# Optimization experiments

Measured on AMD Instinct MI355X. Metric: run time of the kernel, lower is better.

## Reference

```python
import jax, jax.numpy as jnp
import numpy as np

EPS = 0.01       # perturbation radius (constructor arg)
MEAN = 0.1307    # MNIST normalize constants from the 'else' branch
SIGMA = 0.3081


def _get_bound(v, eps):
    # torch get_bound detaches eps before taking |.| and summing
    r = jnp.sum(jnp.abs(jax.lax.stop_gradient(eps)), axis=-1)
    return v + r, v - r


def _relu_zono(v, eps):
    # v: [N], eps: [N, E]. Append one fresh (zero) error column, as the torch code does.
    n = v.shape[0]
    eps = jnp.concatenate([eps, jnp.zeros((n, 1), eps.dtype)], axis=-1)  # [N, E+1]
    u, l = _get_bound(v, eps)
    denom = u - l  # = 2*sum|eps| >= 0; guard against 0 for non-crossing rows
    # slopes are created as Parameters = u/(u-l) on the first pass (detached leaf)
    slope = jax.lax.stop_gradient(u / jnp.where(denom == 0, 1.0, denom))
    # at init slope == base = u/(u-l), so the slope <= base branch is taken
    term = (1.0 - slope) * u * 0.5
    crossing = (u > 0) & (l < 0)
    dead = u <= 0
    # torch uses slope.data * values.data for the linear part, + term (term carries grad)
    v_cross = jax.lax.stop_gradient(slope * v) + term
    v_new = jnp.where(dead, 0.0, jnp.where(crossing, v_cross, v))
    eps_cross = jnp.concatenate([slope[:, None] * eps[:, :-1], term[:, None]], axis=-1)
    eps_new = jnp.where(dead[:, None], 0.0, jnp.where(crossing[:, None], eps_cross, eps))
    return v_new, eps_new


def _forward(inputs, W1, b1, W2, b2, W3, b3):
    # initial zonotope build (faithful to source: values = u + l, radii = values - l = u)
    upper = jnp.minimum(inputs + EPS, 1.0)   # upper - relu(upper - 1)
    lower = jnp.maximum(inputs - EPS, 0.0)   # relu(lower)
    values = upper + lower
    eps = jnp.diag((values - lower).flatten())  # [D, D]
    # Normalize layer (the 'else' branch)
    values = (values - MEAN) / SIGMA
    eps = eps / SIGMA
    # Flatten
    v = values.flatten()
    # Linear -> ReLU -> Linear -> ReLU -> Linear
    v = W1 @ v + b1
    eps = W1 @ eps
    v, eps = _relu_zono(v, eps)
    v = W2 @ v + b2
    eps = W2 @ eps
    v, eps = _relu_zono(v, eps)
    v = W3 @ v + b3
    eps = W3 @ eps
    u, l = _get_bound(v, eps)
    return u, l


def setup_inputs() -> dict:
    key = jax.random.key(0)
    ks = jax.random.split(key, 7)
    D, H, O = 1024, 4096, 10
    inputs = jax.random.uniform(ks[0], (1, 1, 32, 32), jnp.float32)
    W1 = jax.random.normal(ks[1], (H, D), jnp.float32) / np.float32(np.sqrt(D))
    b1 = jax.random.normal(ks[2], (H,), jnp.float32) * 0.01
    W2 = jax.random.normal(ks[3], (H, H), jnp.float32) / np.float32(np.sqrt(H))
    b2 = jax.random.normal(ks[4], (H,), jnp.float32) * 0.01
    W3 = jax.random.normal(ks[5], (O, H), jnp.float32) / np.float32(np.sqrt(H))
    b3 = jax.random.normal(ks[6], (O,), jnp.float32) * 0.01
    return {"inputs": inputs, "W1": W1, "b1": b1, "W2": W2, "b2": b2, "W3": W3, "b3": b3}


def reference(inputs, W1, b1, W2, b2, W3, b3):
    return _forward(inputs, W1, b1, W2, b2, W3, b3)
```

## Files before the change

### kernel.cpp

```cpp
#include <hip/hip_runtime.h>
#include <math.h>

#define ZEPS  0.01f
#define ZMEAN 0.1307f
#define ZSIGMA 0.3081f

constexpr int D = 1024, H = 4096, O = 10;

using short8 = __attribute__((ext_vector_type(8))) short;
using f32x4  = __attribute__((ext_vector_type(4))) float;
typedef unsigned short ushort_t;

__device__ inline unsigned short f2bf(float x) {
    unsigned int u = __float_as_uint(x);
    u += 0x7FFFu + ((u >> 16) & 1u);
    return (unsigned short)(u >> 16);
}
__device__ inline float bf2f(unsigned short h) {
    return __uint_as_float(((unsigned int)h) << 16);
}

__device__ inline unsigned int f2bf2_fast(float a, float b) {
    unsigned int ua = __float_as_uint(a) + 0x8000u;
    unsigned int ub = __float_as_uint(b) + 0x8000u;
    return (ua >> 16) | (ub & 0xFFFF0000u);
}

__device__ inline void gl_lds16(const void* g, void* l) {
    __builtin_amdgcn_global_load_lds(
        (const __attribute__((address_space(1))) unsigned int*)g,
        (__attribute__((address_space(3))) unsigned int*)l, 16, 0, 0);
}

__device__ inline float zval(float xv) {
    float up = fminf(xv + ZEPS, 1.f);
    float lo = fmaxf(xv - ZEPS, 0.f);
    return (up + lo - ZMEAN) / ZSIGMA;
}
__device__ inline float zdia(float xv) {
    return fminf(xv + ZEPS, 1.f) / ZSIGMA;
}

__device__ inline void relu_params(float v, float r, float& vout, float& aout, float& tout) {
    float u = v + r, l = v - r;
    float denom = u - l;
    float slope = u / (denom == 0.f ? 1.f : denom);
    float term = (1.f - slope) * u * 0.5f;
    bool dead = (u <= 0.f);
    bool crossing = (u > 0.f) && (l < 0.f);
    vout = dead ? 0.f : (crossing ? (slope * v + term) : v);
    aout = dead ? 0.f : (crossing ? slope : 1.f);
    tout = (!dead && crossing) ? term : 0.f;
}

__global__ __launch_bounds__(256) void k_layer1(const float* __restrict__ W1, const float* __restrict__ b1,
                                                const float* __restrict__ x,
                                                float* __restrict__ v1p, float* __restrict__ a1,
                                                float* __restrict__ t1) {
    int wid = threadIdx.x >> 6, lane = threadIdx.x & 63;
    int i = blockIdx.x * 4 + wid;
    const float* row = W1 + (size_t)i * D;
    float sv = 0.f, sr = 0.f;
#pragma unroll
    for (int it = 0; it < 4; ++it) {
        int j = it * 256 + lane * 4;
        float4 w = *(const float4*)&row[j];
        float4 xx = *(const float4*)&x[j];
        sv += w.x * zval(xx.x) + w.y * zval(xx.y) + w.z * zval(xx.z) + w.w * zval(xx.w);
        sr += fabsf(w.x) * zdia(xx.x) + fabsf(w.y) * zdia(xx.y) +
              fabsf(w.z) * zdia(xx.z) + fabsf(w.w) * zdia(xx.w);
    }
#pragma unroll
    for (int m = 1; m <= 32; m <<= 1) {
        sv += __shfl_xor(sv, m, 64);
        sr += __shfl_xor(sr, m, 64);
    }
    if (lane == 0) {
        float vo, ao, to;
        relu_params(sv + b1[i], sr, vo, ao, to);
        v1p[i] = vo; a1[i] = ao; t1[i] = to;
    }
}

__global__ __launch_bounds__(256) void k_scaleT(const float* __restrict__ W1, const float* __restrict__ a1,
                                                const float* __restrict__ x,
                                                ushort_t* __restrict__ W1sT) {
    __shared__ float tile[32][33];
    int j0 = blockIdx.x * 32, k0 = blockIdx.y * 32;
    int r = threadIdx.x >> 3;
    int c = (threadIdx.x & 7) * 4;
    float4 w = *(const float4*)&W1[(size_t)(k0 + r) * D + j0 + c];
    float4 xx = *(const float4*)&x[j0 + c];
    float a = a1[k0 + r];
    tile[r][c + 0] = a * w.x * zdia(xx.x);
    tile[r][c + 1] = a * w.y * zdia(xx.y);
    tile[r][c + 2] = a * w.z * zdia(xx.z);
    tile[r][c + 3] = a * w.w * zdia(xx.w);
    __syncthreads();
    ushort4 o;
    o.x = f2bf(tile[c + 0][r]);
    o.y = f2bf(tile[c + 1][r]);
    o.z = f2bf(tile[c + 2][r]);
    o.w = f2bf(tile[c + 3][r]);
    *(ushort4*)&W1sT[(size_t)(j0 + r) * H + k0 + c] = o;
}

#define GBK 64
__global__ __launch_bounds__(256) void k_gemm_mfma(const float* __restrict__ A,
                                                   const ushort_t* __restrict__ B,
                                                   const float* __restrict__ v1p,
                                                   const float* __restrict__ t1,
                                                   ushort_t* __restrict__ C,
                                                   float* __restrict__ vpart,
                                                   float* __restrict__ tpart) {
    const int N = D, K = H;
    __shared__ __align__(16) ushort_t As[2][128 * GBK];
    __shared__ __align__(16) ushort_t Bs[2][128 * GBK];
    __shared__ float vt[2048], tt[2048];
    int b = blockIdx.x;
    int u = b & 7, v = b >> 3;
    int z = u >> 2;
    int y = (u & 3) * 8 + (v >> 3);
    int xb = v & 7;
    int tid = threadIdx.x;
    int wave = tid >> 6, lane = tid & 63;
    int bm = y * 128, bn = xb * 128;
    int kbeg = z * (K / 2);
    ushort_t* Cz = C + (size_t)z * ((size_t)H * D);
    int wm = (wave >> 1) * 64, wn = (wave & 1) * 64;

    int srow = lane >> 3, sc = lane & 7, scp = sc ^ srow;
    int r15 = lane & 15, quad = lane >> 4, key = r15 & 7;
    int rowg = tid >> 3, ch = tid & 7;
    int aswz = ch ^ (rowg & 7);

    const int S = (K / 2) / GBK;

    float4 pa[4][2];
    float sv[4] = {0.f, 0.f, 0.f, 0.f}, st[4] = {0.f, 0.f, 0.f, 0.f};

    auto issueA = [&](int s) {
#pragma unroll
        for (int g = 0; g < 4; ++g) {
            const float* ap = &A[(size_t)(bm + g * 32 + rowg) * K + kbeg + s * GBK + ch * 8];
            pa[g][0] = *(const float4*)ap;
            pa[g][1] = *(const float4*)(ap + 4);
        }
    };
    auto issueB = [&](int s, int buf) {
#pragma unroll
        for (int g = 0; g < 2; ++g) {
            int row = wave * 32 + g * 16;
            (void)row;
        }
#pragma unroll
        for (int g = 0; g < 4; ++g) {
            int row = wave * 32 + g * 8;
            gl_lds16(&B[(size_t)(bn + row + srow) * K + kbeg + s * GBK + scp * 8], &Bs[buf][row * GBK]);
        }
    };
    auto cvtwrite = [&](int s, int buf) {
        if ((s & 7) == xb) {
            const float* vp = &vt[s * 64 + ch * 8];
            const float* tp = &tt[s * 64 + ch * 8];
            float4 v0 = *(const float4*)vp, v1 = *(const float4*)(vp + 4);
            float4 t0 = *(const float4*)tp, t1v = *(const float4*)(tp + 4);
#pragma unroll
            for (int g = 0; g < 4; ++g) {
                sv[g] += pa[g][0].x * v0.x + pa[g][0].y * v0.y + pa[g][0].z * v0.z + pa[g][0].w * v0.w
                       + pa[g][1].x * v1.x + pa[g][1].y * v1.y + pa[g][1].z * v1.z + pa[g][1].w * v1.w;
                st[g] += pa[g][0].x * t0.x + pa[g][0].y * t0.y + pa[g][0].z * t0.z + pa[g][0].w * t0.w
                       + pa[g][1].x * t1v.x + pa[g][1].y * t1v.y + pa[g][1].z * t1v.z + pa[g][1].w * t1v.w;
            }
        }
#pragma unroll
        for (int g = 0; g < 4; ++g) {
            uint4 hh;
            hh.x = f2bf2_fast(pa[g][0].x, pa[g][0].y);
            hh.y = f2bf2_fast(pa[g][0].z, pa[g][0].w);
            hh.z = f2bf2_fast(pa[g][1].x, pa[g][1].y);
            hh.w = f2bf2_fast(pa[g][1].z, pa[g][1].w);
            *(uint4*)&As[buf][(g * 32 + rowg) * GBK + aswz * 8] = hh;
        }
    };

    f32x4 acc[4][4];
#pragma unroll
    for (int p = 0; p < 4; ++p)
#pragma unroll
        for (int q = 0; q < 4; ++q) acc[p][q] = (f32x4){0.f, 0.f, 0.f, 0.f};

    issueA(0);
    issueB(0, 0);
    for (int idx = tid; idx < 512; idx += 256) {
        *(float4*)&vt[idx * 4] = *(const float4*)&v1p[kbeg + idx * 4];
        *(float4*)&tt[idx * 4] = *(const float4*)&t1[kbeg + idx * 4];
    }
    __syncthreads();
    cvtwrite(0, 0);
    __syncthreads();

    for (int s = 0; s < S; ++s) {
        int buf = s & 1, nbuf = buf ^ 1;
        if (s + 1 < S) {
            issueA(s + 1);
            issueB(s + 1, nbuf);
        }
#pragma unroll
        for (int kk = 0; kk < 2; ++kk) {
            short8 af[4], bf[4];
#pragma unroll
            for (int mt = 0; mt < 4; ++mt)
                af[mt] = *(const short8*)&As[buf][(wm + mt * 16 + r15) * GBK + (((kk * 4 + quad) ^ key)) * 8];
#pragma unroll
            for (int nt = 0; nt < 4; ++nt)
                bf[nt] = *(const short8*)&Bs[buf][(wn + nt * 16 + r15) * GBK + (((kk * 4 + quad) ^ key)) * 8];
#pragma unroll
            for (int mt = 0; mt < 4; ++mt)
#pragma unroll
                for (int nt = 0; nt < 4; ++nt)
                    acc[mt][nt] = __builtin_amdgcn_mfma_f32_16x16x32_bf16(af[mt], bf[nt], acc[mt][nt], 0, 0, 0);
        }
        if (s + 1 < S) cvtwrite(s + 1, nbuf);
        __syncthreads();
    }

#pragma unroll
    for (int mt = 0; mt < 4; ++mt) {
        int gr = bm + wm + mt * 16 + quad * 4;
#pragma unroll
        for (int nt = 0; nt < 4; ++nt) {
            int gc = bn + wn + nt * 16 + r15;
            Cz[(size_t)(gr + 0) * N + gc] = f2bf(acc[mt][nt][0]);
            Cz[(size_t)(gr + 1) * N + gc] = f2bf(acc[mt][nt][1]);
            Cz[(size_t)(gr + 2) * N + gc] = f2bf(acc[mt][nt][2]);
            Cz[(size_t)(gr + 3) * N + gc] = f2bf(acc[mt][nt][3]);
        }
    }

#pragma unroll
    for (int g = 0; g < 4; ++g) {
        float a = sv[g], bb = st[g];
        a += __shfl_xor(a, 1, 64); a += __shfl_xor(a, 2, 64); a += __shfl_xor(a, 4, 64);
        bb += __shfl_xor(bb, 1, 64); bb += __shfl_xor(bb, 2, 64); bb += __shfl_xor(bb, 4, 64);
        if (ch == 0) {
            int i = bm + g * 32 + rowg;
            vpart[(size_t)(z * 8 + xb) * H + i] = a;
            tpart[(size_t)(z * 8 + xb) * H + i] = bb;
        }
    }
}

__global__ __launch_bounds__(256) void k_relu2(const ushort_t* __restrict__ e1, const ushort_t* __restrict__ e2,
                                               const float* __restrict__ vpart, const float* __restrict__ tpart,
                                               const float* __restrict__ b2, const float* __restrict__ W3,
                                               float* __restrict__ v2p, float* __restrict__ a2,
                                               float* __restrict__ t2, float* __restrict__ t2col,
                                               float* __restrict__ w3s) {
    int wid = threadIdx.x >> 6, lane = threadIdx.x & 63;
    int i = blockIdx.x * 4 + wid;
    float s = 0.f;
#pragma unroll
    for (int it = 0; it < 2; ++it) {
        int j = lane * 8 + it * 512;
        ushort4 a0 = *(const ushort4*)&e1[(size_t)i * D + j];
        ushort4 a1v = *(const ushort4*)&e1[(size_t)i * D + j + 4];
        ushort4 b0 = *(const ushort4*)&e2[(size_t)i * D + j];
        ushort4 b1v = *(const ushort4*)&e2[(size_t)i * D + j + 4];
        s += fabsf(bf2f(a0.x) + bf2f(b0.x)) + fabsf(bf2f(a0.y) + bf2f(b0.y))
           + fabsf(bf2f(a0.z) + bf2f(b0.z)) + fabsf(bf2f(a0.w) + bf2f(b0.w))
           + fabsf(bf2f(a1v.x) + bf2f(b1v.x)) + fabsf(bf2f(a1v.y) + bf2f(b1v.y))
           + fabsf(bf2f(a1v.z) + bf2f(b1v.z)) + fabsf(bf2f(a1v.w) + bf2f(b1v.w));
    }
    float ve = (lane < 16) ? vpart[(size_t)lane * H + i] : 0.f;
    float te = (lane < 16) ? tpart[(size_t)lane * H + i] : 0.f;
#pragma unroll
    for (int m = 1; m <= 32; m <<= 1) {
        s += __shfl_xor(s, m, 64);
        ve += __shfl_xor(ve, m, 64);
        te += __shfl_xor(te, m, 64);
    }
    float vo, ao, to;
    relu_params(ve + b2[i], s + fabsf(te), vo, ao, to);
    if (lane == 0) { v2p[i] = vo; a2[i] = ao; t2[i] = to; t2col[i] = te; }
    if (lane < O) w3s[(size_t)i * O + lane] = W3[(size_t)lane * H + i] * ao;
}

__global__ __launch_bounds__(256) void k_eps3a(const ushort_t* __restrict__ e1, const ushort_t* __restrict__ e2,
                                               const float* __restrict__ w3s,
                                               float* __restrict__ pbuf) {
    int jb = blockIdx.x, ib = blockIdx.y;
    int jj = threadIdx.x & 15, s = threadIdx.x >> 4;
    int j = jb * 64 + jj * 4;
    int i0 = ib * 128 + s * 8;
    float acc[4][O];
#pragma unroll
    for (int c = 0; c < 4; ++c)
#pragma unroll
        for (int o = 0; o < O; ++o) acc[c][o] = 0.f;
    for (int ii = 0; ii < 8; ++ii) {
        int i = i0 + ii;
        ushort4 a = *(const ushort4*)&e1[(size_t)i * D + j];
        ushort4 b = *(const ushort4*)&e2[(size_t)i * D + j];
        float e0 = bf2f(a.x) + bf2f(b.x), ee1 = bf2f(a.y) + bf2f(b.y);
        float ee2 = bf2f(a.z) + bf2f(b.z), ee3 = bf2f(a.w) + bf2f(b.w);
        const float* w = &w3s[(size_t)i * O];
#pragma unroll
        for (int o = 0; o < O; ++o) {
            float wo = w[o];
            acc[0][o] += wo * e0; acc[1][o] += wo * ee1;
            acc[2][o] += wo * ee2; acc[3][o] += wo * ee3;
        }
    }
    __shared__ float sm[16][64][O];
#pragma unroll
    for (int c = 0; c < 4; ++c)
#pragma unroll
        for (int o = 0; o < O; ++o) sm[s][jj * 4 + c][o] = acc[c][o];
    __syncthreads();
    for (int idx = threadIdx.x; idx < 64 * O; idx += 256) {
        int col = idx / O, o = idx % O;
        float t = 0.f;
#pragma unroll
        for (int ss = 0; ss < 16; ++ss) t += sm[ss][col][o];
        pbuf[((size_t)o * 32 + ib) * D + jb * 64 + col] = t;
    }
}

__global__ __launch_bounds__(256) void k_final(const float* __restrict__ W3, const float* __restrict__ b3,
                                               const float* __restrict__ v2p, const float* __restrict__ a2,
                                               const float* __restrict__ t2col, const float* __restrict__ t2,
                                               const float* __restrict__ pbuf, float* __restrict__ out) {
    int o = blockIdx.x, tid = threadIdx.x;
    float s3 = 0.f;
    for (int j = tid; j < D; j += 256) {
        float t = 0.f;
#pragma unroll
        for (int ib = 0; ib < 32; ++ib) t += pbuf[((size_t)o * 32 + ib) * D + j];
        s3 += fabsf(t);
    }
    const float* row = W3 + (size_t)o * H;
    float sv = 0.f, s1 = 0.f, s2 = 0.f;
    for (int i = tid; i < H; i += 256) {
        float w = row[i];
        sv += w * v2p[i];
        s1 += w * a2[i] * t2col[i];
        s2 += w * t2[i];
    }
    __shared__ float ra[256], rb[256], rc[256], rd[256];
    ra[tid] = sv; rb[tid] = s1; rc[tid] = s2; rd[tid] = s3;
    __syncthreads();
    for (int off = 128; off; off >>= 1) {
        if (tid < off) {
            ra[tid] += ra[tid + off]; rb[tid] += rb[tid + off];
            rc[tid] += rc[tid + off]; rd[tid] += rd[tid + off];
        }
        __syncthreads();
    }
    if (tid == 0) {
        float v3 = ra[0] + b3[o];
        float rr = rd[0] + fabsf(rb[0]) + fabsf(rc[0]);
        out[o] = v3 + rr;
        out[O + o] = v3 - rr;
    }
}

extern "C" void kernel_launch(void* const* d_in, const int* in_sizes, int n_in,
                              void* d_out, int out_size, void* d_ws, size_t ws_size,
                              hipStream_t stream) {
    const float* x  = (const float*)d_in[0];
    const float* W1 = (const float*)d_in[1];
    const float* b1 = (const float*)d_in[2];
    const float* W2 = (const float*)d_in[3];
    const float* b2 = (const float*)d_in[4];
    const float* W3 = (const float*)d_in[5];
    const float* b3 = (const float*)d_in[6];
    float* out = (float*)d_out;

    float* p = (float*)d_ws;
    float* v1p    = p; p += H;
    float* a1     = p; p += H;
    float* t1     = p; p += H;
    float* t2col  = p; p += H;
    float* v2p    = p; p += H;
    float* a2     = p; p += H;
    float* t2     = p; p += H;
    float* w3s    = p; p += H * O + 8;
    float* vpart  = p; p += 16 * H;
    float* tpart  = p; p += 16 * H;
    float* pbuf   = p; p += 32 * O * D;
    ushort_t* eps2  = (ushort_t*)p;
    ushort_t* W1sT  = eps2 + (size_t)2 * H * D;
    ushort_t* eps2b = eps2 + (size_t)H * D;

    k_layer1<<<H / 4, 256, 0, stream>>>(W1, b1, x, v1p, a1, t1);
    k_scaleT<<<dim3(D / 32, H / 32), 256, 0, stream>>>(W1, a1, x, W1sT);
    k_gemm_mfma<<<512, 256, 0, stream>>>(W2, W1sT, v1p, t1, eps2, vpart, tpart);
    k_relu2<<<H / 4, 256, 0, stream>>>(eps2, eps2b, vpart, tpart, b2, W3, v2p, a2, t2, t2col, w3s);
    k_eps3a<<<dim3(D / 64, 32), 256, 0, stream>>>(eps2, eps2b, w3s, pbuf);
    k_final<<<O, 256, 0, stream>>>(W3, b3, v2p, a2, t2col, t2, pbuf, out);
}
```

Baseline: 207.0 us.

## Fuse relu2 and eps3 projection into one kernel reusing eps rows

Merges the second ReLU bound kernel and the W3 projection of eps2 into one kernel. Each block handles 16 rows: it computes the row bounds and slopes, builds scaled W3 weights in shared memory, then projects the same rows (likely still in cache). This removes a launch and a second full pass over eps2 from global memory. In exchange pbuf grows to 256 partials per output, and k_final, now run with 1024 threads, must sum 256 partial rows per column instead of 32.

```diff
diff --git a/kernel.cpp b/kernel.cpp
--- a/kernel.cpp
+++ b/kernel.cpp
@@ -6,9 +6,11 @@
 #define ZSIGMA 0.3081f
 
 constexpr int D = 1024, H = 4096, O = 10;
-
-using short8 = __attribute__((ext_vector_type(8))) short;
-using f32x4  = __attribute__((ext_vector_type(4))) float;
+constexpr size_t HD = (size_t)H * D;
+
+using short8  = __attribute__((ext_vector_type(8))) short;
+using ushort8 = __attribute__((ext_vector_type(8))) unsigned short;
+using f32x4   = __attribute__((ext_vector_type(4))) float;
 typedef unsigned short ushort_t;
 
 __device__ inline unsigned short f2bf(float x) {
@@ -19,7 +21,6 @@
 __device__ inline float bf2f(unsigned short h) {
     return __uint_as_float(((unsigned int)h) << 16);
 }
-
 __device__ inline unsigned int f2bf2_fast(float a, float b) {
     unsigned int ua = __float_as_uint(a) + 0x8000u;
     unsigned int ub = __float_as_uint(b) + 0x8000u;
@@ -126,7 +127,7 @@
     int wave = tid >> 6, lane = tid & 63;
     int bm = y * 128, bn = xb * 128;
     int kbeg = z * (K / 2);
-    ushort_t* Cz = C + (size_t)z * ((size_t)H * D);
+    ushort_t* Cz = C + (size_t)z * HD;
     int wm = (wave >> 1) * 64, wn = (wave & 1) * 64;
 
     int srow = lane >> 3, sc = lane & 7, scp = sc ^ srow;
@@ -148,11 +149,6 @@
         }
     };
     auto issueB = [&](int s, int buf) {
-#pragma unroll
-        for (int g = 0; g < 2; ++g) {
-            int row = wave * 32 + g * 16;
-            (void)row;
-        }
 #pragma unroll
         for (int g = 0; g < 4; ++g) {
             int row = wave * 32 + g * 8;
@@ -251,60 +247,67 @@
     }
 }
 
-__global__ __launch_bounds__(256) void k_relu2(const ushort_t* __restrict__ e1, const ushort_t* __restrict__ e2,
-                                               const float* __restrict__ vpart, const float* __restrict__ tpart,
-                                               const float* __restrict__ b2, const float* __restrict__ W3,
-                                               float* __restrict__ v2p, float* __restrict__ a2,
-                                               float* __restrict__ t2, float* __restrict__ t2col,
-                                               float* __restrict__ w3s) {
-    int wid = threadIdx.x >> 6, lane = threadIdx.x & 63;
-    int i = blockIdx.x * 4 + wid;
-    float s = 0.f;
-#pragma unroll
-    for (int it = 0; it < 2; ++it) {
-        int j = lane * 8 + it * 512;
-        ushort4 a0 = *(const ushort4*)&e1[(size_t)i * D + j];
-        ushort4 a1v = *(const ushort4*)&e1[(size_t)i * D + j + 4];
-        ushort4 b0 = *(const ushort4*)&e2[(size_t)i * D + j];
-        ushort4 b1v = *(const ushort4*)&e2[(size_t)i * D + j + 4];
-        s += fabsf(bf2f(a0.x) + bf2f(b0.x)) + fabsf(bf2f(a0.y) + bf2f(b0.y))
-           + fabsf(bf2f(a0.z) + bf2f(b0.z)) + fabsf(bf2f(a0.w) + bf2f(b0.w))
-           + fabsf(bf2f(a1v.x) + bf2f(b1v.x)) + fabsf(bf2f(a1v.y) + bf2f(b1v.y))
-           + fabsf(bf2f(a1v.z) + bf2f(b1v.z)) + fabsf(bf2f(a1v.w) + bf2f(b1v.w));
-    }
-    float ve = (lane < 16) ? vpart[(size_t)lane * H + i] : 0.f;
-    float te = (lane < 16) ? tpart[(size_t)lane * H + i] : 0.f;
-#pragma unroll
-    for (int m = 1; m <= 32; m <<= 1) {
-        s += __shfl_xor(s, m, 64);
-        ve += __shfl_xor(ve, m, 64);
-        te += __shfl_xor(te, m, 64);
-    }
-    float vo, ao, to;
-    relu_params(ve + b2[i], s + fabsf(te), vo, ao, to);
-    if (lane == 0) { v2p[i] = vo; a2[i] = ao; t2[i] = to; t2col[i] = te; }
-    if (lane < O) w3s[(size_t)i * O + lane] = W3[(size_t)lane * H + i] * ao;
-}
-
-__global__ __launch_bounds__(256) void k_eps3a(const ushort_t* __restrict__ e1, const ushort_t* __restrict__ e2,
-                                               const float* __restrict__ w3s,
-                                               float* __restrict__ pbuf) {
-    int jb = blockIdx.x, ib = blockIdx.y;
-    int jj = threadIdx.x & 15, s = threadIdx.x >> 4;
-    int j = jb * 64 + jj * 4;
-    int i0 = ib * 128 + s * 8;
+__global__ __launch_bounds__(256) void k_mid(const ushort_t* __restrict__ e1, const ushort_t* __restrict__ e2,
+                                             const float* __restrict__ vpart, const float* __restrict__ tpart,
+                                             const float* __restrict__ b2, const float* __restrict__ W3,
+                                             float* __restrict__ v2p, float* __restrict__ a2,
+                                             float* __restrict__ t2, float* __restrict__ t2col,
+                                             float* __restrict__ pbuf) {
+    __shared__ float sa2[16];
+    __shared__ float sw3[16][O];
+    int blk = blockIdx.x, tid = threadIdx.x;
+    int wave = tid >> 6, lane = tid & 63;
+
+#pragma unroll
+    for (int r = 0; r < 4; ++r) {
+        int ii = wave * 4 + r;
+        int i = blk * 16 + ii;
+        size_t off = (size_t)i * D + lane * 16;
+        ushort8 a0 = *(const ushort8*)&e1[off];
+        ushort8 a1v = *(const ushort8*)&e1[off + 8];
+        ushort8 b0 = *(const ushort8*)&e2[off];
+        ushort8 b1v = *(const ushort8*)&e2[off + 8];
+        float s = 0.f;
+#pragma unroll
+        for (int q = 0; q < 8; ++q)
+            s += fabsf(bf2f(a0[q]) + bf2f(b0[q])) + fabsf(bf2f(a1v[q]) + bf2f(b1v[q]));
+        float ve = (lane < 16) ? vpart[(size_t)lane * H + i] : 0.f;
+        float te = (lane < 16) ? tpart[(size_t)lane * H + i] : 0.f;
+#pragma unroll
+        for (int m = 1; m <= 32; m <<= 1) {
+            s += __shfl_xor(s, m, 64);
+            ve += __shfl_xor(ve, m, 64);
+            te += __shfl_xor(te, m, 64);
+        }
+        if (lane == 0) {
+            float vo, ao, to;
+            relu_params(ve + b2[i], s + fabsf(te), vo, ao, to);
+            v2p[i] = vo; a2[i] = ao; t2[i] = to; t2col[i] = te; sa2[ii] = ao;
+        }
+    }
+    __syncthreads();
+    if (tid < 16 * O) {
+        int ii = tid / O, o = tid % O;
+        sw3[ii][o] = W3[(size_t)o * H + blk * 16 + ii] * sa2[ii];
+    }
+    __syncthreads();
+
+    int j = tid * 4;
     float acc[4][O];
 #pragma unroll
     for (int c = 0; c < 4; ++c)
 #pragma unroll
         for (int o = 0; o < O; ++o) acc[c][o] = 0.f;
-    for (int ii = 0; ii < 8; ++ii) {
-        int i = i0 + ii;
-        ushort4 a = *(const ushort4*)&e1[(size_t)i * D + j];
-        ushort4 b = *(const ushort4*)&e2[(size_t)i * D + j];
-        float e0 = bf2f(a.x) + bf2f(b.x), ee1 = bf2f(a.y) + bf2f(b.y);
-        float ee2 = bf2f(a.z) + bf2f(b.z), ee3 = bf2f(a.w) + bf2f(b.w);
-        const float* w = &w3s[(size_t)i * O];
+#pragma unroll
+    for (int ii = 0; ii < 16; ++ii) {
+        size_t off = (size_t)(blk * 16 + ii) * D + j;
+        ushort4 za = *(const ushort4*)&e1[off];
+        ushort4 zb = *(const ushort4*)&e2[off];
+        float e0 = bf2f(za.x) + bf2f(zb.x);
+        float ee1 = bf2f(za.y) + bf2f(zb.y);
+        float ee2 = bf2f(za.z) + bf2f(zb.z);
+        float ee3 = bf2f(za.w) + bf2f(zb.w);
+        const float* w = sw3[ii];
 #pragma unroll
         for (int o = 0; o < O; ++o) {
             float wo = w[o];
@@ -312,54 +315,48 @@
             acc[2][o] += wo * ee2; acc[3][o] += wo * ee3;
         }
     }
-    __shared__ float sm[16][64][O];
-#pragma unroll
-    for (int c = 0; c < 4; ++c)
-#pragma unroll
-        for (int o = 0; o < O; ++o) sm[s][jj * 4 + c][o] = acc[c][o];
-    __syncthreads();
-    for (int idx = threadIdx.x; idx < 64 * O; idx += 256) {
-        int col = idx / O, o = idx % O;
-        float t = 0.f;
-#pragma unroll
-        for (int ss = 0; ss < 16; ++ss) t += sm[ss][col][o];
-        pbuf[((size_t)o * 32 + ib) * D + jb * 64 + col] = t;
-    }
-}
-
-__global__ __launch_bounds__(256) void k_final(const float* __restrict__ W3, const float* __restrict__ b3,
-                                               const float* __restrict__ v2p, const float* __restrict__ a2,
-                                               const float* __restrict__ t2col, const float* __restrict__ t2,
-                                               const float* __restrict__ pbuf, float* __restrict__ out) {
+#pragma unroll
+    for (int o = 0; o < O; ++o) {
+        float4 stv = make_float4(acc[0][o], acc[1][o], acc[2][o], acc[3][o]);
+        *(float4*)&pbuf[((size_t)o * 256 + blk) * D + j] = stv;
+    }
+}
+
+__global__ __launch_bounds__(1024) void k_final(const float* __restrict__ W3, const float* __restrict__ b3,
+                                                const float* __restrict__ v2p, const float* __restrict__ a2,
+                                                const float* __restrict__ t2col, const float* __restrict__ t2,
+                                                const float* __restrict__ pbuf, float* __restrict__ out) {
     int o = blockIdx.x, tid = threadIdx.x;
-    float s3 = 0.f;
-    for (int j = tid; j < D; j += 256) {
-        float t = 0.f;
-#pragma unroll
-        for (int ib = 0; ib < 32; ++ib) t += pbuf[((size_t)o * 32 + ib) * D + j];
-        s3 += fabsf(t);
-    }
+    float t = 0.f;
+    const float* pb = pbuf + (size_t)o * 256 * D;
+    for (int s = 0; s < 256; ++s) t += pb[(size_t)s * D + tid];
+    float s3 = fabsf(t);
+
     const float* row = W3 + (size_t)o * H;
     float sv = 0.f, s1 = 0.f, s2 = 0.f;
-    for (int i = tid; i < H; i += 256) {
+#pragma unroll
+    for (int it = 0; it < 4; ++it) {
+        int i = it * 1024 + tid;
         float w = row[i];
         sv += w * v2p[i];
         s1 += w * a2[i] * t2col[i];
         s2 += w * t2[i];
     }
-    __shared__ float ra[256], rb[256], rc[256], rd[256];
-    ra[tid] = sv; rb[tid] = s1; rc[tid] = s2; rd[tid] = s3;
-    __syncthreads();
-    for (int off = 128; off; off >>= 1) {
-        if (tid < off) {
-            ra[tid] += ra[tid + off]; rb[tid] += rb[tid + off];
-            rc[tid] += rc[tid + off]; rd[tid] += rd[tid + off];
+    __shared__ float red[4][1024];
+    red[0][tid] = sv; red[1][tid] = s1; red[2][tid] = s2; red[3][tid] = s3;
+    __syncthreads();
+    for (int off2 = 512; off2; off2 >>= 1) {
+        if (tid < off2) {
+            red[0][tid] += red[0][tid + off2];
+            red[1][tid] += red[1][tid + off2];
+            red[2][tid] += red[2][tid + off2];
+            red[3][tid] += red[3][tid + off2];
         }
         __syncthreads();
     }
     if (tid == 0) {
-        float v3 = ra[0] + b3[o];
-        float rr = rd[0] + fabsf(rb[0]) + fabsf(rc[0]);
+        float v3 = red[0][0] + b3[o];
+        float rr = red[3][0] + fabsf(red[1][0]) + fabsf(red[2][0]);
         out[o] = v3 + rr;
         out[O + o] = v3 - rr;
     }
@@ -378,25 +375,23 @@
     float* out = (float*)d_out;
 
     float* p = (float*)d_ws;
-    float* v1p    = p; p += H;
-    float* a1     = p; p += H;
-    float* t1     = p; p += H;
-    float* t2col  = p; p += H;
-    float* v2p    = p; p += H;
-    float* a2     = p; p += H;
-    float* t2     = p; p += H;
-    float* w3s    = p; p += H * O + 8;
-    float* vpart  = p; p += 16 * H;
-    float* tpart  = p; p += 16 * H;
-    float* pbuf   = p; p += 32 * O * D;
-    ushort_t* eps2  = (ushort_t*)p;
-    ushort_t* W1sT  = eps2 + (size_t)2 * H * D;
-    ushort_t* eps2b = eps2 + (size_t)H * D;
+    float* v1p   = p; p += H;
+    float* a1    = p; p += H;
+    float* t1    = p; p += H;
+    float* t2col = p; p += H;
+    float* v2p   = p; p += H;
+    float* a2    = p; p += H;
+    float* t2    = p; p += H;
+    float* vpart = p; p += 16 * H;
+    float* tpart = p; p += 16 * H;
+    float* pbuf  = p; p += (size_t)O * 256 * D;
+    ushort_t* eps2 = (ushort_t*)p;
+    ushort_t* W1sT = eps2 + 2 * HD;
+    ushort_t* eps2b = eps2 + HD;
 
     k_layer1<<<H / 4, 256, 0, stream>>>(W1, b1, x, v1p, a1, t1);
     k_scaleT<<<dim3(D / 32, H / 32), 256, 0, stream>>>(W1, a1, x, W1sT);
     k_gemm_mfma<<<512, 256, 0, stream>>>(W2, W1sT, v1p, t1, eps2, vpart, tpart);
-    k_relu2<<<H / 4, 256, 0, stream>>>(eps2, eps2b, vpart, tpart, b2, W3, v2p, a2, t2, t2col, w3s);
-    k_eps3a<<<dim3(D / 64, 32), 256, 0, stream>>>(eps2, eps2b, w3s, pbuf);
-    k_final<<<O, 256, 0, stream>>>(W3, b3, v2p, a2, t2col, t2, pbuf, out);
-}
+    k_mid<<<256, 256, 0, stream>>>(eps2, eps2b, vpart, tpart, b2, W3, v2p, a2, t2, t2col, pbuf);
+    k_final<<<O, 1024, 0, stream>>>(W3, b3, v2p, a2, t2col, t2, pbuf, out);
+}
```

After: 210.0 us. Within noise of the previous version (+1.5%).
